# Optimization experiments

Measured on AMD Instinct MI355X. Metric: run time of the kernel, lower is better.

Reference implementation:

```python
import jax, jax.numpy as jnp
import numpy as np

N_LAYERS = 3
HEADS = 2
HID = 64
IN_DIM = 10
NEG_SLOPE = 0.2  # DGL EGATConv leaky_relu default
B, NPG = 8, 6250  # batch_size, nodes per graph (== max_n_nodes)
N = B * NPG
E = 500000
N_RES = 30  # max_n_resources


def _mlp2(x, W0, b0, W1, b1):
    return jax.nn.relu(x @ W0 + b0) @ W1 + b1


def _segment_softmax(e, dst, n):
    # softmax over incoming edges of each destination node (DGL edge_softmax)
    m = jax.ops.segment_max(e, dst, num_segments=n)
    m = jnp.where(jnp.isfinite(m), m, 0.0)
    ex = jnp.exp(e - m[dst])
    s = jax.ops.segment_sum(ex, dst, num_segments=n)
    return ex / (s[dst] + 1e-9)


def _egat(h, f, src, dst, W_ni, W_nj, W_fij, W_node, attn, bias):
    # per-edge attention features: f_ni[src] + f_nj[dst] + f_fij + bias
    f_out = (h @ W_ni)[src] + (h @ W_nj)[dst] + f @ W_fij + bias   # (E, H*HID)
    f_out = jax.nn.leaky_relu(f_out, NEG_SLOPE).reshape(-1, HEADS, HID)
    e = (f_out * attn[None]).sum(-1)                               # (E, H)
    alpha = _segment_softmax(e, dst, h.shape[0])
    msg = alpha[:, :, None] * (h @ W_node).reshape(-1, HEADS, HID)[src]
    h_out = jax.ops.segment_sum(msg, dst, num_segments=h.shape[0])  # (N, H, HID)
    return h_out, f_out


def _forward(feat, att_rc, att_rp, etype_emb, rid_emb, rc_W, rc_b, rp_W, rp_b,
             fe_W0, fe_b0, fe_W1, fe_b1,
             W_ni, W_nj, W_fij, W_node, attn, egat_bias,
             Wm0, bm0, Wm1, bm1, src, dst, etype, rid):
    feats_list = [feat]
    h = _mlp2(feat, fe_W0, fe_b0, fe_W1, fe_b1)
    feats_list.append(h)
    # 'sum' edge embedding flavor
    emb = etype_emb[etype] + rid_emb[rid] + (att_rc @ rc_W + rc_b) + (att_rp @ rp_W + rp_b)
    for l in range(N_LAYERS):
        h_att, _ = _egat(h, emb, src, dst, W_ni[l], W_nj[l], W_fij[l], W_node[l],
                         attn[l], egat_bias[l])
        h = _mlp2(h_att.reshape(-1, HEADS * HID), Wm0[l], bm0[l], Wm1[l], bm1[l]) + feats_list[-1]
        feats_list.append(h)
    features = jnp.concatenate(feats_list, axis=1)       # (N, IN_DIM + HID*(L+1))
    node_features = features.reshape(B, NPG, -1)
    graph_embedding = node_features.max(axis=1)          # graph_pooling='max'
    rep = jnp.broadcast_to(graph_embedding[:, None, :], node_features.shape)
    return jnp.concatenate([node_features, rep], axis=2)  # (B, NPG, 2*F)


def setup_inputs():
    key = jax.random.key(0)
    ks = iter(jax.random.split(key, 40))
    def rn(shape, s=0.1):
        return jax.random.normal(next(ks), shape, dtype=jnp.float32) * s
    HO = HEADS * HID
    inp = {}
    inp['feat'] = rn((N, IN_DIM), 1.0)
    inp['att_rc'] = rn((E, 2), 1.0)
    inp['att_rp'] = rn((E, 3), 1.0)
    inp['etype_emb'] = rn((7, HID))
    inp['rid_emb'] = rn((N_RES + 1, HID))
    inp['rc_W'] = rn((2, HID)); inp['rc_b'] = rn((HID,))
    inp['rp_W'] = rn((3, HID)); inp['rp_b'] = rn((HID,))
    inp['fe_W0'] = rn((IN_DIM, HID)); inp['fe_b0'] = rn((HID,))
    inp['fe_W1'] = rn((HID, HID)); inp['fe_b1'] = rn((HID,))
    inp['W_ni'] = rn((N_LAYERS, HID, HO)); inp['W_nj'] = rn((N_LAYERS, HID, HO))
    inp['W_fij'] = rn((N_LAYERS, HID, HO)); inp['W_node'] = rn((N_LAYERS, HID, HO))
    inp['attn'] = rn((N_LAYERS, HEADS, HID)); inp['egat_bias'] = rn((N_LAYERS, HO))
    inp['Wm0'] = rn((N_LAYERS, HO, HO)); inp['bm0'] = rn((N_LAYERS, HO))
    inp['Wm1'] = rn((N_LAYERS, HO, HID)); inp['bm1'] = rn((N_LAYERS, HID))
    inp['src'] = jax.random.randint(next(ks), (E,), 0, N, dtype=jnp.int32)
    inp['dst'] = jax.random.randint(next(ks), (E,), 0, N, dtype=jnp.int32)
    inp['etype'] = jax.random.randint(next(ks), (E,), 0, 7, dtype=jnp.int32)
    inp['rid'] = jax.random.randint(next(ks), (E,), 0, N_RES + 1, dtype=jnp.int32)
    return inp


def reference(feat, att_rc, att_rp, etype_emb, rid_emb, rc_W, rc_b, rp_W, rp_b,
              fe_W0, fe_b0, fe_W1, fe_b1, W_ni, W_nj, W_fij, W_node, attn, egat_bias,
              Wm0, bm0, Wm1, bm1, src, dst, etype, rid):
    return _forward(feat, att_rc, att_rp, etype_emb, rid_emb, rc_W, rc_b, rp_W, rp_b,
                    fe_W0, fe_b0, fe_W1, fe_b1, W_ni, W_nj, W_fij, W_node, attn, egat_bias,
                    Wm0, bm0, Wm1, bm1, src, dst, etype, rid)
```

## Files before the change

### kernel.cpp

```cpp
#include <hip/hip_runtime.h>
#include <hip/hip_bf16.h>
#include <math.h>

#define N_NODES 50000
#define N_EDGES 500000
#define B_GRAPHS 8
#define NPG 6250
#define HID 64
#define HO 128
#define IN_DIM 10
#define F_TOT 266
#define OUT_C 532
#define NEG_SLOPE 0.2f
#define NT_ROWS 44
#define SCB 200
#define SCH 250

typedef short bf16x8 __attribute__((ext_vector_type(8)));
typedef float f32x4 __attribute__((ext_vector_type(4)));

__device__ __forceinline__ float LD(const void* p, size_t i, int f32) {
    if (f32) return ((const float*)p)[i];
    unsigned u = ((const unsigned short*)p)[i];
    return __uint_as_float(u << 16);
}
__device__ __forceinline__ unsigned fkey(float f) {
    unsigned b = __float_as_uint(f);
    return (b & 0x80000000u) ? ~b : (b | 0x80000000u);
}
__device__ __forceinline__ float funkey(unsigned k) {
    unsigned b = (k & 0x80000000u) ? (k & 0x7fffffffu) : ~k;
    return __uint_as_float(b);
}
__device__ __forceinline__ unsigned short rnebf(float x) {
    unsigned u = __float_as_uint(x);
    return (unsigned short)((u + 0x7FFFu + ((u >> 16) & 1u)) >> 16);
}
__device__ __forceinline__ unsigned pk2(float lo, float hi) {
    return (unsigned)rnebf(lo) | ((unsigned)rnebf(hi) << 16);
}
__device__ __forceinline__ float plo(unsigned u) { return __uint_as_float(u << 16); }
__device__ __forceinline__ float phi(unsigned u) { return __uint_as_float(u & 0xFFFF0000u); }
__device__ __forceinline__ float wsum(float x) {
    x += __int_as_float(__builtin_amdgcn_update_dpp(0, __float_as_int(x), 0xB1, 0xF, 0xF, true));
    x += __int_as_float(__builtin_amdgcn_update_dpp(0, __float_as_int(x), 0x4E, 0xF, 0xF, true));
    x += __int_as_float(__builtin_amdgcn_update_dpp(0, __float_as_int(x), 0x141, 0xF, 0xF, true));
    x += __int_as_float(__builtin_amdgcn_update_dpp(0, __float_as_int(x), 0x140, 0xF, 0xF, true));
    x += __shfl_xor(x, 16, 64);
    x += __shfl_xor(x, 32, 64);
    return x;
}

__global__ void k_detect(const void* __restrict__ att_rc, int* __restrict__ flagp) {
    __shared__ int cnt;
    if (threadIdx.x == 0) cnt = 0;
    __syncthreads();
    const unsigned short* w = (const unsigned short*)att_rc;
    int c = 0;
    for (int i = threadIdx.x; i < 8192; i += 256) {
        unsigned e = (w[i] >> 7) & 0xFF;
        if (e >= 0xC0) c++;
    }
    atomicAdd(&cnt, c);
    __syncthreads();
    if (threadIdx.x == 0) *flagp = (cnt > 8) ? 1 : 0;
}

__global__ void k_wprep(const void* __restrict__ W_ni, const void* __restrict__ W_nj,
                        const void* __restrict__ W_node, const void* __restrict__ Wm0,
                        const void* __restrict__ Wm1,
                        unsigned short* __restrict__ pw_n,
                        unsigned short* __restrict__ pw_m0,
                        unsigned short* __restrict__ pw_m1,
                        const int* __restrict__ flagp) {
    const int f32 = *flagp;
    int i = blockIdx.x * 256 + threadIdx.x;
    if (i < 73728) {
        int k = i & 63, c = (i >> 6) & 127, lm = i >> 13;
        int m = lm % 3, l = lm / 3;
        const void* W = (m == 0) ? W_ni : (m == 1) ? W_nj : W_node;
        pw_n[i] = rnebf(LD(W, (size_t)l * 8192 + k * 128 + c, f32));
    } else if (i < 73728 + 49152) {
        int j = i - 73728;
        int k = j & 127, c = (j >> 7) & 127, l = j >> 14;
        pw_m0[j] = rnebf(LD(Wm0, (size_t)l * 16384 + k * 128 + c, f32));
    } else if (i < 147456) {
        int j = i - 122880;
        int k = j & 127, c = (j >> 7) & 63, l = j >> 13;
        pw_m1[j] = rnebf(LD(Wm1, (size_t)l * 8192 + k * 64 + c, f32));
    }
}

__global__ void k_count(const int* __restrict__ dst, int* __restrict__ cnt) {
    int i = blockIdx.x * blockDim.x + threadIdx.x;
    int stride = gridDim.x * blockDim.x;
    for (int e = i; e < N_EDGES; e += stride) atomicAdd(&cnt[dst[e]], 1);
}

__global__ void k_scan1(const int* __restrict__ cnt, int* __restrict__ bsum) {
    __shared__ int red[256];
    int b = blockIdx.x, t = threadIdx.x;
    red[t] = (t < SCH) ? cnt[b * SCH + t] : 0;
    __syncthreads();
    for (int off = 128; off; off >>= 1) {
        if (t < off) red[t] += red[t + off];
        __syncthreads();
    }
    if (t == 0) bsum[b] = red[0];
}
__global__ void k_scan2(const int* __restrict__ bsum, int* __restrict__ boff) {
    __shared__ int ts[256];
    int t = threadIdx.x;
    int v = (t < SCB) ? bsum[t] : 0;
    ts[t] = v;
    __syncthreads();
    for (int off = 1; off < 256; off <<= 1) {
        int u = (t >= off) ? ts[t - off] : 0;
        __syncthreads();
        ts[t] += u;
        __syncthreads();
    }
    if (t < SCB) boff[t] = ts[t] - v;
}
__global__ void k_scan3(const int* __restrict__ cnt, const int* __restrict__ boff,
                        int* __restrict__ rowptr, int* __restrict__ cursor) {
    __shared__ int ts[256];
    int b = blockIdx.x, t = threadIdx.x;
    int base = b * SCH;
    int v = (t < SCH) ? cnt[base + t] : 0;
    ts[t] = v;
    __syncthreads();
    for (int off = 1; off < 256; off <<= 1) {
        int u = (t >= off) ? ts[t - off] : 0;
        __syncthreads();
        ts[t] += u;
        __syncthreads();
    }
    if (t < SCH) {
        int r = boff[b] + ts[t] - v;
        rowptr[base + t] = r;
        cursor[base + t] = r;
    }
    if (b == SCB - 1 && t == SCH - 1) rowptr[N_NODES] = boff[b] + ts[t];
}

__global__ void k_fill(const int* __restrict__ src, const int* __restrict__ dst,
                       const int* __restrict__ etype, const int* __restrict__ rid,
                       const void* __restrict__ att_rc, const void* __restrict__ att_rp,
                       int* __restrict__ cursor, uint4* __restrict__ emeta,
                       const int* __restrict__ flagp) {
    const int f32 = *flagp;
    int i = blockIdx.x * blockDim.x + threadIdx.x;
    int stride = gridDim.x * blockDim.x;
    for (int e = i; e < N_EDGES; e += stride) {
        int d = dst[e];
        int j = atomicAdd(&cursor[d], 1);
        float rc0 = LD(att_rc, 2 * (size_t)e, f32), rc1 = LD(att_rc, 2 * (size_t)e + 1, f32);
        float rp0 = LD(att_rp, 3 * (size_t)e, f32), rp1 = LD(att_rp, 3 * (size_t)e + 1, f32),
              rp2 = LD(att_rp, 3 * (size_t)e + 2, f32);
        uint4 m;
        m.x = pk2(rc0, rc1);
        m.y = pk2(rp0, rp1);
        m.z = pk2(rp2, 0.f);
        m.w = (unsigned)(etype[e] | (rid[e] << 3) | ((unsigned)src[e] << 8));
        emeta[j] = m;
    }
}

__global__ void k_init(const void* __restrict__ feat,
                       const void* __restrict__ W0, const void* __restrict__ b0,
                       const void* __restrict__ W1, const void* __restrict__ b1,
                       float* __restrict__ feats, const int* __restrict__ flagp) {
    const int f32 = *flagp;
    __shared__ float sf[64 * 12];
    __shared__ float sW0[IN_DIM * 64];
    __shared__ float sb0[64], sb1[64];
    __shared__ float sh[64 * 64];
    __shared__ float sW1[64 * 64];
    int tid = threadIdx.x, n0 = blockIdx.x * 64;
    for (int i = tid; i < IN_DIM * 64; i += 256) sW0[i] = LD(W0, i, f32);
    for (int i = tid; i < 64; i += 256) { sb0[i] = LD(b0, i, f32); sb1[i] = LD(b1, i, f32); }
    for (int i = tid; i < 64 * 64; i += 256) sW1[i] = LD(W1, i, f32);
    for (int i = tid; i < 64 * IN_DIM; i += 256) {
        int n = n0 + i / IN_DIM, c = i % IN_DIM;
        sf[(i / IN_DIM) * 12 + c] = (n < N_NODES) ? LD(feat, (size_t)n * IN_DIM + c, f32) : 0.f;
    }
    __syncthreads();
    int ng = tid / 16, cg = tid % 16;
    float acc[4][4];
    #pragma unroll
    for (int i = 0; i < 4; i++)
        #pragma unroll
        for (int j = 0; j < 4; j++) acc[i][j] = sb0[cg * 4 + j];
    #pragma unroll
    for (int k = 0; k < IN_DIM; k++)
        #pragma unroll
        for (int i = 0; i < 4; i++) {
            float a = sf[(ng * 4 + i) * 12 + k];
            #pragma unroll
            for (int j = 0; j < 4; j++) acc[i][j] += a * sW0[k * 64 + cg * 4 + j];
        }
    #pragma unroll
    for (int i = 0; i < 4; i++)
        #pragma unroll
        for (int j = 0; j < 4; j++) sh[(ng * 4 + i) * 64 + cg * 4 + j] = fmaxf(acc[i][j], 0.f);
    __syncthreads();
    float o[4][4];
    #pragma unroll
    for (int i = 0; i < 4; i++)
        #pragma unroll
        for (int j = 0; j < 4; j++) o[i][j] = sb1[cg * 4 + j];
    for (int k = 0; k < 64; k++) {
        float4 bv = *(const float4*)&sW1[k * 64 + cg * 4];
        #pragma unroll
        for (int i = 0; i < 4; i++) {
            float a = sh[(ng * 4 + i) * 64 + k];
            o[i][0] += a * bv.x; o[i][1] += a * bv.y;
            o[i][2] += a * bv.z; o[i][3] += a * bv.w;
        }
    }
    #pragma unroll
    for (int i = 0; i < 4; i++) {
        int n = n0 + ng * 4 + i;
        if (n < N_NODES) {
            float* r = feats + (size_t)n * F_TOT;
            #pragma unroll
            for (int j = 0; j < 4; j++) r[IN_DIM + cg * 4 + j] = o[i][j];
        }
    }
    for (int i = tid; i < 64 * IN_DIM; i += 256) {
        int n = n0 + i / IN_DIM, c = i % IN_DIM;
        if (n < N_NODES) feats[(size_t)n * F_TOT + c] = sf[(i / IN_DIM) * 12 + c];
    }
}

__global__ void k_tables(const void* __restrict__ etype_emb, const void* __restrict__ rid_emb,
                         const void* __restrict__ rc_W, const void* __restrict__ rc_b,
                         const void* __restrict__ rp_W, const void* __restrict__ rp_b,
                         const void* __restrict__ W_fij, const void* __restrict__ egat_bias,
                         float* __restrict__ T, const int* __restrict__ flagp) {
    const int f32 = *flagp;
    int l = blockIdx.x;
    __shared__ float S[NT_ROWS * HID];
    __shared__ float W[HID * HO];
    for (int i = threadIdx.x; i < 7 * HID; i += 256) S[i] = LD(etype_emb, i, f32);
    for (int i = threadIdx.x; i < 31 * HID; i += 256) S[7 * HID + i] = LD(rid_emb, i, f32);
    for (int i = threadIdx.x; i < 2 * HID; i += 256) S[38 * HID + i] = LD(rc_W, i, f32);
    for (int i = threadIdx.x; i < 3 * HID; i += 256) S[40 * HID + i] = LD(rp_W, i, f32);
    for (int i = threadIdx.x; i < HID; i += 256)
        S[43 * HID + i] = LD(rc_b, i, f32) + LD(rp_b, i, f32);
    for (int i = threadIdx.x; i < HID * HO; i += 256)
        W[i] = LD(W_fij, (size_t)l * HID * HO + i, f32);
    __syncthreads();
    for (int idx = threadIdx.x; idx < NT_ROWS * HO; idx += 256) {
        int r = idx / HO, c = idx % HO;
        float acc = (r == 43) ? LD(egat_bias, l * HO + c, f32) : 0.f;
        for (int k = 0; k < HID; k++) acc += S[r * HID + k] * W[k * HO + c];
        T[(size_t)l * NT_ROWS * HO + idx] = acc;
    }
}

__global__ void __launch_bounds__(256) k_ngemm(
        const float* __restrict__ feats, int h_off,
        const unsigned short* __restrict__ pw_n, int l,
        unsigned* __restrict__ gsrc, unsigned* __restrict__ gdst) {
    __shared__ __align__(16) unsigned short Xs[64 * 72];
    __shared__ __align__(16) unsigned short Ws[384 * 72];
    int tid = threadIdx.x, n0 = blockIdx.x * 64;
    for (int i = tid; i < 64 * 64; i += 256) {
        int n = i >> 6, c = i & 63, gn = n0 + n;
        Xs[n * 72 + c] = rnebf((gn < N_NODES) ? feats[(size_t)gn * F_TOT + h_off + c] : 0.f);
    }
    const uint4* pn = (const uint4*)pw_n + (size_t)l * 3072;
    for (int i = tid; i < 3072; i += 256) {
        int kq = i & 7, mc = i >> 3;
        *(uint4*)&Ws[mc * 72 + kq * 8] = pn[i];
    }
    __syncthreads();
    int wid = tid >> 6, lane = tid & 63;
    int row0 = wid * 16, mrow = lane & 15, quad = lane >> 4;
    bf16x8 a0 = *(const bf16x8*)&Xs[(row0 + mrow) * 72 + quad * 8];
    bf16x8 a1 = *(const bf16x8*)&Xs[(row0 + mrow) * 72 + 32 + quad * 8];
    f32x4 accA[8], accB[8];
    #pragma unroll
    for (int j = 0; j < 8; j++) { accA[j] = (f32x4){0,0,0,0}; accB[j] = (f32x4){0,0,0,0}; }
    #pragma unroll
    for (int j = 0; j < 8; j++) {
        bf16x8 b0 = *(const bf16x8*)&Ws[(0 * 128 + j * 16 + mrow) * 72 + quad * 8];
        bf16x8 b1 = *(const bf16x8*)&Ws[(0 * 128 + j * 16 + mrow) * 72 + 32 + quad * 8];
        accA[j] = __builtin_amdgcn_mfma_f32_16x16x32_bf16(a0, b0, accA[j], 0, 0, 0);
        accA[j] = __builtin_amdgcn_mfma_f32_16x16x32_bf16(a1, b1, accA[j], 0, 0, 0);
        bf16x8 c0 = *(const bf16x8*)&Ws[(2 * 128 + j * 16 + mrow) * 72 + quad * 8];
        bf16x8 c1 = *(const bf16x8*)&Ws[(2 * 128 + j * 16 + mrow) * 72 + 32 + quad * 8];
        accB[j] = __builtin_amdgcn_mfma_f32_16x16x32_bf16(a0, c0, accB[j], 0, 0, 0);
        accB[j] = __builtin_amdgcn_mfma_f32_16x16x32_bf16(a1, c1, accB[j], 0, 0, 0);
    }
    #pragma unroll
    for (int j = 0; j < 4; j++) {
        int c = j * 16 + mrow;
        #pragma unroll
        for (int r = 0; r < 4; r++) {
            int gn = n0 + row0 + quad * 4 + r;
            if (gn < N_NODES) {
                uint2 v;
                v.x = pk2(accA[j][r], accA[j + 4][r]);
                v.y = pk2(accB[j][r], accB[j + 4][r]);
                *(uint2*)&gsrc[(size_t)gn * 128 + c * 2] = v;
            }
        }
    }
    f32x4 accC[8];
    #pragma unroll
    for (int j = 0; j < 8; j++) accC[j] = (f32x4){0,0,0,0};
    #pragma unroll
    for (int j = 0; j < 8; j++) {
        bf16x8 b0 = *(const bf16x8*)&Ws[(1 * 128 + j * 16 + mrow) * 72 + quad * 8];
        bf16x8 b1 = *(const bf16x8*)&Ws[(1 * 128 + j * 16 + mrow) * 72 + 32 + quad * 8];
        accC[j] = __builtin_amdgcn_mfma_f32_16x16x32_bf16(a0, b0, accC[j], 0, 0, 0);
        accC[j] = __builtin_amdgcn_mfma_f32_16x16x32_bf16(a1, b1, accC[j], 0, 0, 0);
    }
    #pragma unroll
    for (int j = 0; j < 4; j++) {
        int c = j * 16 + mrow;
        #pragma unroll
        for (int r = 0; r < 4; r++) {
            int gn = n0 + row0 + quad * 4 + r;
            if (gn < N_NODES)
                gdst[(size_t)gn * 64 + c] = pk2(accC[j][r], accC[j + 4][r]);
        }
    }
}

__global__ void __launch_bounds__(256) k_edge_fused(
        const float* __restrict__ T, const void* __restrict__ attn, int l,
        const unsigned* __restrict__ gsrc, const unsigned* __restrict__ gdst,
        const int* __restrict__ rowptr, const uint4* __restrict__ emeta,
        float* __restrict__ h_att, const int* __restrict__ flagp) {
    const int f32 = *flagp;
    __shared__ float Ts[38 * HO];
    const float* Tl = T + (size_t)l * NT_ROWS * HO;
    for (int i4 = threadIdx.x; i4 < 38 * HO / 4; i4 += 256)
        ((float4*)Ts)[i4] = ((const float4*)Tl)[i4];
    int lane = threadIdx.x & 63;
    float C0[6], C1[6];
    #pragma unroll
    for (int r = 0; r < 6; r++) {
        C0[r] = Tl[(38 + r) * HO + lane];
        C1[r] = Tl[(38 + r) * HO + 64 + lane];
    }
    float AT0 = LD(attn, l * HO + lane, f32), AT1 = LD(attn, l * HO + 64 + lane, f32);
    __syncthreads();
    int d = blockIdx.x * 4 + (threadIdx.x >> 6);
    int jb = rowptr[d], je = rowptr[d + 1];
    unsigned gd = gdst[(size_t)d * 64 + lane];
    float nj0 = plo(gd) + C0[5], nj1 = phi(gd) + C1[5];
    float l0 = 0.f, a0 = 0.f, l1 = 0.f, a1 = 0.f;

    auto logits = [&](const uint4& em, const uint2& g,
                      float& e0, float& e1, float& h0, float& h1) {
        unsigned w = em.w;
        int et = (int)(w & 7u), ri = (int)((w >> 3) & 31u);
        float rc0 = plo(em.x), rc1 = phi(em.x);
        float rp0 = plo(em.y), rp1 = phi(em.y), rp2 = plo(em.z);
        float ni0 = plo(g.x), ni1 = phi(g.x);
        h0 = plo(g.y); h1 = phi(g.y);
        float x0 = ni0 + nj0 + Ts[et * HO + lane] + Ts[(7 + ri) * HO + lane]
                 + rc0 * C0[0] + rc1 * C0[1] + rp0 * C0[2] + rp1 * C0[3] + rp2 * C0[4];
        float x1 = ni1 + nj1 + Ts[et * HO + 64 + lane] + Ts[(7 + ri) * HO + 64 + lane]
                 + rc0 * C1[0] + rc1 * C1[1] + rp0 * C1[2] + rp1 * C1[3] + rp2 * C1[4];
        x0 = (x0 > 0.f) ? x0 : NEG_SLOPE * x0;
        x1 = (x1 > 0.f) ? x1 : NEG_SLOPE * x1;
        e0 = wsum(x0 * AT0);
        e1 = wsum(x1 * AT1);
    };
    auto update = [&](float e0, float e1, float h0, float h1) {
        float w0 = __expf(e0), w1 = __expf(e1);
        l0 += w0; a0 = fmaf(w0, h0, a0);
        l1 += w1; a1 = fmaf(w1, h1, a1);
    };
    auto fetch = [&](int j, uint4& em, uint2& g) {
        em = emeta[j];
        g = *(const uint2*)&gsrc[(size_t)(em.w >> 8) * 128 + lane * 2];
    };

    uint4 emA = make_uint4(0,0,0,0), emB = make_uint4(0,0,0,0);
    uint2 gA = make_uint2(0,0), gB = make_uint2(0,0);
    int j = jb;
    if (j < je)     fetch(j, emA, gA);
    if (j + 1 < je) fetch(j + 1, emB, gB);
    while (j + 2 <= je) {
        float e0a, e1a, h0a, h1a, e0b, e1b, h0b, h1b;
        logits(emA, gA, e0a, e1a, h0a, h1a);
        logits(emB, gB, e0b, e1b, h0b, h1b);
        if (j + 2 < je) fetch(j + 2, emA, gA);
        if (j + 3 < je) fetch(j + 3, emB, gB);
        update(e0a, e1a, h0a, h1a);
        update(e0b, e1b, h0b, h1b);
        j += 2;
    }
    if (j < je) {
        float e0, e1, h0, h1;
        logits(emA, gA, e0, e1, h0, h1);
        update(e0, e1, h0, h1);
    }
    h_att[(size_t)d * HO + lane]      = a0 / (l0 + 1e-9f);
    h_att[(size_t)d * HO + 64 + lane] = a1 / (l1 + 1e-9f);
}

__global__ void __launch_bounds__(256) k_mlp(
        const float* __restrict__ h_att,
        const unsigned short* __restrict__ pw_m0, const void* __restrict__ bm0,
        const unsigned short* __restrict__ pw_m1, const void* __restrict__ bm1, int l,
        float* __restrict__ feats, int prev_off, int out_off,
        const int* __restrict__ flagp) {
    const int f32 = *flagp;
    __shared__ __align__(16) unsigned short Xs[64 * 136];
    __shared__ __align__(16) unsigned short W0T[128 * 136];
    __shared__ __align__(16) unsigned short W1T[64 * 136];
    __shared__ float sb0[HO], sb1[64];
    int tid = threadIdx.x, n0 = blockIdx.x * 64;
    for (int i = tid; i < 64 * 128; i += 256) {
        int n = i >> 7, c = i & 127, gn = n0 + n;
        Xs[n * 136 + c] = rnebf((gn < N_NODES) ? h_att[(size_t)gn * HO + c] : 0.f);
    }
    const uint4* p0 = (const uint4*)pw_m0 + (size_t)l * 2048;
    for (int i = tid; i < 2048; i += 256) {
        int kq = i & 15, c = i >> 4;
        *(uint4*)&W0T[c * 136 + kq * 8] = p0[i];
    }
    const uint4* p1 = (const uint4*)pw_m1 + (size_t)l * 1024;
    for (int i = tid; i < 1024; i += 256) {
        int kq = i & 15, c = i >> 4;
        *(uint4*)&W1T[c * 136 + kq * 8] = p1[i];
    }
    for (int i = tid; i < HO; i += 256) sb0[i] = LD(bm0, l * HO + i, f32);
    for (int i = tid; i < 64; i += 256) sb1[i] = LD(bm1, l * 64 + i, f32);
    __syncthreads();
    int wid = tid >> 6, lane = tid & 63;
    int row0 = wid * 16, mrow = lane & 15, quad = lane >> 4;
    f32x4 acc[8];
    #pragma unroll
    for (int j = 0; j < 8; j++) {
        float b = sb0[j * 16 + mrow];
        acc[j] = (f32x4){b, b, b, b};
    }
    #pragma unroll
    for (int ks = 0; ks < 4; ks++) {
        bf16x8 a = *(const bf16x8*)&Xs[(row0 + mrow) * 136 + ks * 32 + quad * 8];
        #pragma unroll
        for (int j = 0; j < 8; j++) {
            bf16x8 b = *(const bf16x8*)&W0T[(j * 16 + mrow) * 136 + ks * 32 + quad * 8];
            acc[j] = __builtin_amdgcn_mfma_f32_16x16x32_bf16(a, b, acc[j], 0, 0, 0);
        }
    }
    #pragma unroll
    for (int j = 0; j < 8; j++)
        #pragma unroll
        for (int r = 0; r < 4; r++)
            Xs[(row0 + quad * 4 + r) * 136 + j * 16 + mrow] = rnebf(fmaxf(acc[j][r], 0.f));
    f32x4 o[4];
    #pragma unroll
    for (int j = 0; j < 4; j++) {
        float b = sb1[j * 16 + mrow];
        o[j] = (f32x4){b, b, b, b};
    }
    #pragma unroll
    for (int ks = 0; ks < 4; ks++) {
        bf16x8 a = *(const bf16x8*)&Xs[(row0 + mrow) * 136 + ks * 32 + quad * 8];
        #pragma unroll
        for (int j = 0; j < 4; j++) {
            bf16x8 b = *(const bf16x8*)&W1T[(j * 16 + mrow) * 136 + ks * 32 + quad * 8];
            o[j] = __builtin_amdgcn_mfma_f32_16x16x32_bf16(a, b, o[j], 0, 0, 0);
        }
    }
    #pragma unroll
    for (int j = 0; j < 4; j++) {
        int c = j * 16 + mrow;
        #pragma unroll
        for (int r = 0; r < 4; r++) {
            int gn = n0 + row0 + quad * 4 + r;
            if (gn < N_NODES) {
                float* rw = feats + (size_t)gn * F_TOT;
                rw[out_off + c] = o[j][r] + rw[prev_off + c];
            }
        }
    }
}

__global__ void k_pool(const float* __restrict__ feats, unsigned* __restrict__ gmax) {
    int g = blockIdx.x;
    int chunk = blockIdx.y;
    int t = threadIdx.x;
    const int CS = 49;
    int nb = chunk * CS;
    int ne = (nb + CS < NPG) ? nb + CS : NPG;
    float m0 = -INFINITY, m1 = -INFINITY;
    for (int n = nb; n < ne; n++) {
        const float* row = feats + (size_t)(g * NPG + n) * F_TOT;
        m0 = fmaxf(m0, row[t]);
        if (t + 256 < F_TOT) m1 = fmaxf(m1, row[t + 256]);
    }
    atomicMax(&gmax[g * F_TOT + t], fkey(m0));
    if (t + 256 < F_TOT) atomicMax(&gmax[g * F_TOT + t + 256], fkey(m1));
}

__global__ void k_out(const float* __restrict__ feats, const unsigned* __restrict__ gmax,
                      void* __restrict__ out, const int* __restrict__ flagp) {
    const int f32 = *flagp;
    int lane = threadIdx.x & 63;
    int wave = (blockIdx.x * blockDim.x + threadIdx.x) >> 6;
    int nw = (gridDim.x * blockDim.x) >> 6;
    for (int row = wave; row < B_GRAPHS * NPG; row += nw) {
        int g = row / NPG;
        const float* fr = feats + (size_t)row * F_TOT;
        const unsigned* gr = gmax + g * F_TOT;
        if (f32) {
            float* o = (float*)out + (size_t)row * OUT_C;
            for (int c = lane; c < OUT_C; c += 64)
                o[c] = (c < F_TOT) ? fr[c] : funkey(gr[c - F_TOT]);
        } else {
            __hip_bfloat16* o = (__hip_bfloat16*)out + (size_t)row * OUT_C;
            for (int c = lane; c < OUT_C; c += 64)
                o[c] = __float2bfloat16((c < F_TOT) ? fr[c] : funkey(gr[c - F_TOT]));
        }
    }
}

extern "C" void kernel_launch(void* const* d_in, const int* in_sizes, int n_in,
                              void* d_out, int out_size, void* d_ws, size_t ws_size,
                              hipStream_t stream) {
    const void* feat      = d_in[0];
    const void* att_rc    = d_in[1];
    const void* att_rp    = d_in[2];
    const void* etype_emb = d_in[3];
    const void* rid_emb   = d_in[4];
    const void* rc_W      = d_in[5];
    const void* rc_b      = d_in[6];
    const void* rp_W      = d_in[7];
    const void* rp_b      = d_in[8];
    const void* fe_W0     = d_in[9];
    const void* fe_b0     = d_in[10];
    const void* fe_W1     = d_in[11];
    const void* fe_b1     = d_in[12];
    const void* W_ni      = d_in[13];
    const void* W_nj      = d_in[14];
    const void* W_fij     = d_in[15];
    const void* W_node    = d_in[16];
    const void* attn      = d_in[17];
    const void* egat_bias = d_in[18];
    const void* Wm0       = d_in[19];
    const void* bm0       = d_in[20];
    const void* Wm1       = d_in[21];
    const void* bm1       = d_in[22];
    const int* src   = (const int*)d_in[23];
    const int* dst   = (const int*)d_in[24];
    const int* etype = (const int*)d_in[25];
    const int* rid   = (const int*)d_in[26];

    char* p = (char*)d_ws;
    auto alloc = [&](size_t bytes) {
        char* r = p;
        p += (bytes + 255) & ~(size_t)255;
        return r;
    };
    float*    feats  = (float*)alloc((size_t)N_NODES * F_TOT * 4);
    unsigned* gsrc   = (unsigned*)alloc((size_t)N_NODES * HO * 4);
    unsigned* gdst   = (unsigned*)alloc((size_t)N_NODES * 64 * 4);
    float*    h_att  = (float*)alloc((size_t)N_NODES * HO * 4);
    float*    T      = (float*)alloc((size_t)3 * NT_ROWS * HO * 4);
    unsigned* gmax   = (unsigned*)alloc((size_t)B_GRAPHS * F_TOT * 4);
    int*      flagp  = (int*)alloc(256);
    int*      rowptr = (int*)alloc((size_t)(N_NODES + 1) * 4);
    int*      cursor = (int*)alloc((size_t)N_NODES * 4);
    int*      cnt    = (int*)alloc((size_t)N_NODES * 4);
    int*      bsum   = (int*)alloc((size_t)SCB * 4);
    int*      boff   = (int*)alloc((size_t)SCB * 4);
    uint4*    emeta  = (uint4*)alloc((size_t)N_EDGES * 16);
    unsigned short* pw_n  = (unsigned short*)alloc((size_t)73728 * 2);
    unsigned short* pw_m0 = (unsigned short*)alloc((size_t)49152 * 2);
    unsigned short* pw_m1 = (unsigned short*)alloc((size_t)24576 * 2);

    k_detect<<<1, 256, 0, stream>>>(att_rc, flagp);
    hipMemsetAsync(cnt, 0, (size_t)N_NODES * 4, stream);
    hipMemsetAsync(gmax, 0, (size_t)B_GRAPHS * F_TOT * 4, stream);
    k_wprep<<<576, 256, 0, stream>>>(W_ni, W_nj, W_node, Wm0, Wm1,
                                     pw_n, pw_m0, pw_m1, flagp);
    k_count<<<512, 256, 0, stream>>>(dst, cnt);
    k_scan1<<<SCB, 256, 0, stream>>>(cnt, bsum);
    k_scan2<<<1, 256, 0, stream>>>(bsum, boff);
    k_scan3<<<SCB, 256, 0, stream>>>(cnt, boff, rowptr, cursor);
    k_fill<<<1024, 256, 0, stream>>>(src, dst, etype, rid, att_rc, att_rp,
                                     cursor, emeta, flagp);
    k_init<<<(N_NODES + 63) / 64, 256, 0, stream>>>(feat, fe_W0, fe_b0, fe_W1, fe_b1,
                                                    feats, flagp);
    k_tables<<<3, 256, 0, stream>>>(etype_emb, rid_emb, rc_W, rc_b, rp_W, rp_b,
                                    W_fij, egat_bias, T, flagp);
    for (int l = 0; l < 3; l++) {
        int h_off = IN_DIM + l * HID;
        int out_off = IN_DIM + (l + 1) * HID;
        k_ngemm<<<(N_NODES + 63) / 64, 256, 0, stream>>>(feats, h_off, pw_n, l, gsrc, gdst);
        k_edge_fused<<<N_NODES / 4, 256, 0, stream>>>(T, attn, l, gsrc, gdst,
                                                      rowptr, emeta, h_att, flagp);
        k_mlp<<<(N_NODES + 63) / 64, 256, 0, stream>>>(h_att, pw_m0, bm0, pw_m1, bm1, l,
                                                       feats, h_off, out_off, flagp);
    }
    k_pool<<<dim3(B_GRAPHS, 128), 256, 0, stream>>>(feats, gmax);
    k_out<<<2048, 256, 0, stream>>>(feats, gmax, d_out, flagp);
}
```

Baseline: 813.2 us.

## Pack edge-attention math into float2, merge head reductions, two nodes per wave

Rewrites the fused edge-attention kernel so the two heads are handled as packed float2 values, allowing packed FP32 arithmetic. The two per-head wave reductions become one: a permlane32 swap combines the halves, a single DPP/swizzle reduction runs, and a second swap redistributes the results. Each wave now processes two destination nodes and the grid is halved, spreading the shared-memory table load over more work. The cost is sequential per-wave processing of two nodes, which may reduce latency hiding on the irregular gathers.

```diff
diff --git a/kernel.cpp b/kernel.cpp
--- a/kernel.cpp
+++ b/kernel.cpp
@@ -18,6 +18,7 @@
 
 typedef short bf16x8 __attribute__((ext_vector_type(8)));
 typedef float f32x4 __attribute__((ext_vector_type(4)));
+typedef float f32x2 __attribute__((ext_vector_type(2)));
 
 __device__ __forceinline__ float LD(const void* p, size_t i, int f32) {
     if (f32) return ((const float*)p)[i];
@@ -41,14 +42,8 @@
 }
 __device__ __forceinline__ float plo(unsigned u) { return __uint_as_float(u << 16); }
 __device__ __forceinline__ float phi(unsigned u) { return __uint_as_float(u & 0xFFFF0000u); }
-__device__ __forceinline__ float wsum(float x) {
-    x += __int_as_float(__builtin_amdgcn_update_dpp(0, __float_as_int(x), 0xB1, 0xF, 0xF, true));
-    x += __int_as_float(__builtin_amdgcn_update_dpp(0, __float_as_int(x), 0x4E, 0xF, 0xF, true));
-    x += __int_as_float(__builtin_amdgcn_update_dpp(0, __float_as_int(x), 0x141, 0xF, 0xF, true));
-    x += __int_as_float(__builtin_amdgcn_update_dpp(0, __float_as_int(x), 0x140, 0xF, 0xF, true));
-    x += __shfl_xor(x, 16, 64);
-    x += __shfl_xor(x, 32, 64);
-    return x;
+__device__ __forceinline__ f32x2 up2(unsigned u) {
+    return (f32x2){__uint_as_float(u << 16), __uint_as_float(u & 0xFFFF0000u)};
 }
 
 __global__ void k_detect(const void* __restrict__ att_rc, int* __restrict__ flagp) {
@@ -337,74 +332,92 @@
         const int* __restrict__ rowptr, const uint4* __restrict__ emeta,
         float* __restrict__ h_att, const int* __restrict__ flagp) {
     const int f32 = *flagp;
-    __shared__ float Ts[38 * HO];
+    __shared__ f32x2 Ts2[38 * 64];
     const float* Tl = T + (size_t)l * NT_ROWS * HO;
-    for (int i4 = threadIdx.x; i4 < 38 * HO / 4; i4 += 256)
-        ((float4*)Ts)[i4] = ((const float4*)Tl)[i4];
-    int lane = threadIdx.x & 63;
-    float C0[6], C1[6];
-    #pragma unroll
-    for (int r = 0; r < 6; r++) {
-        C0[r] = Tl[(38 + r) * HO + lane];
-        C1[r] = Tl[(38 + r) * HO + 64 + lane];
-    }
-    float AT0 = LD(attn, l * HO + lane, f32), AT1 = LD(attn, l * HO + 64 + lane, f32);
-    __syncthreads();
-    int d = blockIdx.x * 4 + (threadIdx.x >> 6);
-    int jb = rowptr[d], je = rowptr[d + 1];
-    unsigned gd = gdst[(size_t)d * 64 + lane];
-    float nj0 = plo(gd) + C0[5], nj1 = phi(gd) + C1[5];
-    float l0 = 0.f, a0 = 0.f, l1 = 0.f, a1 = 0.f;
-
-    auto logits = [&](const uint4& em, const uint2& g,
-                      float& e0, float& e1, float& h0, float& h1) {
-        unsigned w = em.w;
-        int et = (int)(w & 7u), ri = (int)((w >> 3) & 31u);
-        float rc0 = plo(em.x), rc1 = phi(em.x);
-        float rp0 = plo(em.y), rp1 = phi(em.y), rp2 = plo(em.z);
-        float ni0 = plo(g.x), ni1 = phi(g.x);
-        h0 = plo(g.y); h1 = phi(g.y);
-        float x0 = ni0 + nj0 + Ts[et * HO + lane] + Ts[(7 + ri) * HO + lane]
-                 + rc0 * C0[0] + rc1 * C0[1] + rp0 * C0[2] + rp1 * C0[3] + rp2 * C0[4];
-        float x1 = ni1 + nj1 + Ts[et * HO + 64 + lane] + Ts[(7 + ri) * HO + 64 + lane]
-                 + rc0 * C1[0] + rc1 * C1[1] + rp0 * C1[2] + rp1 * C1[3] + rp2 * C1[4];
-        x0 = (x0 > 0.f) ? x0 : NEG_SLOPE * x0;
-        x1 = (x1 > 0.f) ? x1 : NEG_SLOPE * x1;
-        e0 = wsum(x0 * AT0);
-        e1 = wsum(x1 * AT1);
-    };
-    auto update = [&](float e0, float e1, float h0, float h1) {
-        float w0 = __expf(e0), w1 = __expf(e1);
-        l0 += w0; a0 = fmaf(w0, h0, a0);
-        l1 += w1; a1 = fmaf(w1, h1, a1);
-    };
-    auto fetch = [&](int j, uint4& em, uint2& g) {
-        em = emeta[j];
-        g = *(const uint2*)&gsrc[(size_t)(em.w >> 8) * 128 + lane * 2];
-    };
-
-    uint4 emA = make_uint4(0,0,0,0), emB = make_uint4(0,0,0,0);
-    uint2 gA = make_uint2(0,0), gB = make_uint2(0,0);
-    int j = jb;
-    if (j < je)     fetch(j, emA, gA);
-    if (j + 1 < je) fetch(j + 1, emB, gB);
-    while (j + 2 <= je) {
-        float e0a, e1a, h0a, h1a, e0b, e1b, h0b, h1b;
-        logits(emA, gA, e0a, e1a, h0a, h1a);
-        logits(emB, gB, e0b, e1b, h0b, h1b);
-        if (j + 2 < je) fetch(j + 2, emA, gA);
-        if (j + 3 < je) fetch(j + 3, emB, gB);
-        update(e0a, e1a, h0a, h1a);
-        update(e0b, e1b, h0b, h1b);
-        j += 2;
-    }
-    if (j < je) {
-        float e0, e1, h0, h1;
-        logits(emA, gA, e0, e1, h0, h1);
-        update(e0, e1, h0, h1);
-    }
-    h_att[(size_t)d * HO + lane]      = a0 / (l0 + 1e-9f);
-    h_att[(size_t)d * HO + 64 + lane] = a1 / (l1 + 1e-9f);
+    int tid = threadIdx.x;
+    for (int i = tid; i < 38 * 64; i += 256) {
+        int r = i >> 6, c = i & 63;
+        Ts2[i] = (f32x2){Tl[r * HO + c], Tl[r * HO + 64 + c]};
+    }
+    int lane = tid & 63;
+    f32x2 C2[6];
+    #pragma unroll
+    for (int r = 0; r < 6; r++)
+        C2[r] = (f32x2){Tl[(38 + r) * HO + lane], Tl[(38 + r) * HO + 64 + lane]};
+    f32x2 AT2 = (f32x2){LD(attn, l * HO + lane, f32), LD(attn, l * HO + 64 + lane, f32)};
+    __syncthreads();
+    int wid = tid >> 6;
+    int d0 = blockIdx.x * 8 + wid * 2;
+
+    #pragma unroll 1
+    for (int dn = 0; dn < 2; dn++) {
+        int d = d0 + dn;
+        int jb = rowptr[d], je = rowptr[d + 1];
+        unsigned gd = gdst[(size_t)d * 64 + lane];
+        f32x2 NJ2 = up2(gd) + C2[5];
+        f32x2 L2 = (f32x2){0.f, 0.f}, A2 = (f32x2){0.f, 0.f};
+
+        auto logits = [&](const uint4& em, const uint2& g, f32x2& e2, f32x2& h2) {
+            unsigned w = em.w;
+            int et = (int)(w & 7u), ri = (int)((w >> 3) & 31u);
+            f32x2 x = up2(g.x) + NJ2;
+            x += Ts2[et * 64 + lane];
+            x += Ts2[(7 + ri) * 64 + lane];
+            x += plo(em.x) * C2[0];
+            x += phi(em.x) * C2[1];
+            x += plo(em.y) * C2[2];
+            x += phi(em.y) * C2[3];
+            x += plo(em.z) * C2[4];
+            f32x2 xs = x * NEG_SLOPE;
+            x.x = fmaxf(x.x, xs.x);
+            x.y = fmaxf(x.y, xs.y);
+            f32x2 p = x * AT2;
+            h2 = up2(g.y);
+            float pa = p.x, pb = p.y;
+            asm("v_permlane32_swap_b32 %0, %1" : "+v"(pa), "+v"(pb));
+            float s = pa + pb;
+            s += __int_as_float(__builtin_amdgcn_update_dpp(0, __float_as_int(s), 0xB1, 0xF, 0xF, true));
+            s += __int_as_float(__builtin_amdgcn_update_dpp(0, __float_as_int(s), 0x4E, 0xF, 0xF, true));
+            s += __int_as_float(__builtin_amdgcn_update_dpp(0, __float_as_int(s), 0x141, 0xF, 0xF, true));
+            s += __int_as_float(__builtin_amdgcn_update_dpp(0, __float_as_int(s), 0x140, 0xF, 0xF, true));
+            s += __int_as_float(__builtin_amdgcn_ds_swizzle(__float_as_int(s), 0x401F));
+            float sa = s, sb = s;
+            asm("v_permlane32_swap_b32 %0, %1" : "+v"(sa), "+v"(sb));
+            e2 = (f32x2){sa, sb};
+        };
+        auto update = [&](f32x2 e2, f32x2 h2) {
+            f32x2 w2 = (f32x2){__expf(e2.x), __expf(e2.y)};
+            L2 += w2;
+            A2 += w2 * h2;
+        };
+        auto fetch = [&](int j, uint4& em, uint2& g) {
+            em = emeta[j];
+            g = *(const uint2*)&gsrc[(size_t)(em.w >> 8) * 128 + lane * 2];
+        };
+
+        uint4 emA = make_uint4(0,0,0,0), emB = make_uint4(0,0,0,0);
+        uint2 gA = make_uint2(0,0), gB = make_uint2(0,0);
+        int j = jb;
+        if (j < je)     fetch(j, emA, gA);
+        if (j + 1 < je) fetch(j + 1, emB, gB);
+        while (j + 2 <= je) {
+            f32x2 eA, hA, eB, hB;
+            logits(emA, gA, eA, hA);
+            logits(emB, gB, eB, hB);
+            if (j + 2 < je) fetch(j + 2, emA, gA);
+            if (j + 3 < je) fetch(j + 3, emB, gB);
+            update(eA, hA);
+            update(eB, hB);
+            j += 2;
+        }
+        if (j < je) {
+            f32x2 e2, h2;
+            logits(emA, gA, e2, h2);
+            update(e2, h2);
+        }
+        h_att[(size_t)d * HO + lane]      = A2.x / (L2.x + 1e-9f);
+        h_att[(size_t)d * HO + 64 + lane] = A2.y / (L2.y + 1e-9f);
+    }
 }
 
 __global__ void __launch_bounds__(256) k_mlp(
@@ -599,7 +612,7 @@
         int h_off = IN_DIM + l * HID;
         int out_off = IN_DIM + (l + 1) * HID;
         k_ngemm<<<(N_NODES + 63) / 64, 256, 0, stream>>>(feats, h_off, pw_n, l, gsrc, gdst);
-        k_edge_fused<<<N_NODES / 4, 256, 0, stream>>>(T, attn, l, gsrc, gdst,
+        k_edge_fused<<<N_NODES / 8, 256, 0, stream>>>(T, attn, l, gsrc, gdst,
                                                       rowptr, emeta, h_att, flagp);
         k_mlp<<<(N_NODES + 63) / 64, 256, 0, stream>>>(h_att, pw_m0, bm0, pw_m1, bm1, l,
                                                        feats, h_off, out_off, flagp);
```

Measured after the change: 797.9 us. No clear change (-1.9%).
